# Kernel optimization log

Hardware: AMD Instinct MI355X
Metric: run time of the kernel (lower is better)

The kernel has to match this reference:

```python
import jax, jax.numpy as jnp
import numpy as np

L = 8192
E = 1024
H = 16
D = E // H  # head_dim = 64


def setup_inputs() -> dict:
    key = jax.random.key(0)
    ks = jax.random.split(key, 5)
    x = jax.random.normal(ks[0], (L, E), dtype=jnp.float32)
    in_proj_weight = jax.random.normal(ks[1], (3 * E, E), dtype=jnp.float32) * (1.0 / np.sqrt(E))
    in_proj_bias = jax.random.normal(ks[2], (3 * E,), dtype=jnp.float32) * 0.02
    out_proj_weight = jax.random.normal(ks[3], (E, E), dtype=jnp.float32) * (1.0 / np.sqrt(E))
    out_proj_bias = jax.random.normal(ks[4], (E,), dtype=jnp.float32) * 0.02
    return {
        "x": x,
        "in_proj_weight": in_proj_weight,
        "in_proj_bias": in_proj_bias,
        "out_proj_weight": out_proj_weight,
        "out_proj_bias": out_proj_bias,
    }


def reference(x, in_proj_weight, in_proj_bias, out_proj_weight, out_proj_bias):
    # Single-token query (decode-style): q from x[:1], k/v from full sequence.
    q = x[:1] @ in_proj_weight[:E].T + in_proj_bias[:E]            # [1, E]
    k = x @ in_proj_weight[E:2 * E].T + in_proj_bias[E:2 * E]      # [L, E]
    v = x @ in_proj_weight[2 * E:].T + in_proj_bias[2 * E:]        # [L, E]

    q = q.reshape(1, H, D).transpose(1, 0, 2)   # [H, 1, D]
    k = k.reshape(L, H, D).transpose(1, 2, 0)   # [H, D, L]
    v = v.reshape(L, H, D).transpose(1, 0, 2)   # [H, L, D]

    scale = 1.0 / np.sqrt(D).astype(np.float32)
    dot = jnp.matmul(q, k) * scale              # [H, 1, L]
    attn = jax.nn.softmax(dot, axis=-1)
    out = jnp.matmul(attn, v)                   # [H, 1, D]
    out = out.transpose(1, 0, 2).reshape(1, E)  # [1, E]
    return out @ out_proj_weight.T + out_proj_bias
```

## Files before the change

### kernel.cpp

```cpp
#include <hip/hip_runtime.h>
#include <hip/hip_bf16.h>

#define LSEQ 8192
#define E 1024
#define H 16

typedef __attribute__((ext_vector_type(8))) short short8;
typedef __attribute__((ext_vector_type(4))) float f32x4;

__device__ inline unsigned short f2bf(float f) {
    union { float f; unsigned int i; } v; v.f = f;
    unsigned int x = v.i;
    unsigned int r = (x + 0x7fffu + ((x >> 16) & 1u)) >> 16;
    return (unsigned short)r;
}

__device__ inline float wave_reduce_sum(float v) {
    #pragma unroll
    for (int off = 32; off > 0; off >>= 1) v += __shfl_xor(v, off, 64);
    return v;
}

__global__ __launch_bounds__(256) void k0_q(
    const float* __restrict__ x, const float* __restrict__ W,
    const float* __restrict__ bias, float* __restrict__ q_ws)
{
    int wave = threadIdx.x >> 6, lane = threadIdx.x & 63;
    int i = blockIdx.x * 4 + wave;
    const f32x4* wp = (const f32x4*)(W + i * E) + lane * 4;
    const f32x4* xp = (const f32x4*)(x) + lane * 4;
    float s = 0.f;
    #pragma unroll
    for (int j = 0; j < 4; j++) {
        f32x4 w4 = wp[j], x4 = xp[j];
        s += w4[0] * x4[0] + w4[1] * x4[1] + w4[2] * x4[2] + w4[3] * x4[3];
    }
    s = wave_reduce_sum(s);
    if (lane == 0) q_ws[i] = s + bias[i];
}

__global__ __launch_bounds__(256) void k1_rc(
    const float* __restrict__ W, const float* __restrict__ bias,
    const float* __restrict__ q_ws, unsigned short* __restrict__ r_bf,
    float* __restrict__ c_ws)
{
    __shared__ float red[4][64];
    int hb = blockIdx.x >> 4, ec = blockIdx.x & 15;
    int lane = threadIdx.x & 63, wq = threadIdx.x >> 6;
    int e = ec * 64 + lane;
    const float* qh = q_ws + hb * 64;
    float acc = 0.f;
    #pragma unroll
    for (int i = 0; i < 16; i++) {
        int d = wq * 16 + i;
        acc += qh[d] * W[(E + hb * 64 + d) * E + e];
    }
    red[wq][lane] = acc;
    __syncthreads();
    if (wq == 0) {
        float s = red[0][lane] + red[1][lane] + red[2][lane] + red[3][lane];
        r_bf[hb * E + e] = f2bf(s * 0.125f);
    }
    if (ec == 0 && wq == 1) {
        float v = qh[lane] * bias[E + hb * 64 + lane];
        v = wave_reduce_sum(v);
        if (lane == 0) c_ws[hb] = v * 0.125f;
    }
}

__global__ __launch_bounds__(256) void k2_scores(
    const float* __restrict__ x,
    const unsigned short* __restrict__ r_bf,
    const float* __restrict__ c_ws,
    float* __restrict__ scores)
{
    __shared__ f32x4 comb[2][64];
    int tid = threadIdx.x;
    int wave = tid >> 6, lane = tid & 63;
    int mloc = wave >> 1, khalf = wave & 1;
    int mtile = blockIdx.x * 2 + mloc;
    int mbase = mtile * 16;
    int rw = lane & 15, quad = lane >> 4;
    float cv = (khalf == 0) ? c_ws[rw] : 0.f;
    f32x4 acc = {cv, cv, cv, cv};
    const f32x4* ap = (const f32x4*)(x + (mbase + rw) * E + khalf * 512) + quad * 2;
    const short8* bp = (const short8*)(r_bf + rw * E + khalf * 512) + quad;
    #pragma unroll 4
    for (int kk = 0; kk < 16; kk++) {
        f32x4 a0 = ap[kk * 8];
        f32x4 a1 = ap[kk * 8 + 1];
        short8 af;
        af[0] = (short)f2bf(a0[0]); af[1] = (short)f2bf(a0[1]);
        af[2] = (short)f2bf(a0[2]); af[3] = (short)f2bf(a0[3]);
        af[4] = (short)f2bf(a1[0]); af[5] = (short)f2bf(a1[1]);
        af[6] = (short)f2bf(a1[2]); af[7] = (short)f2bf(a1[3]);
        short8 bfr = bp[kk * 4];
        acc = __builtin_amdgcn_mfma_f32_16x16x32_bf16(af, bfr, acc, 0, 0, 0);
    }
    if (khalf == 1) comb[mloc][lane] = acc;
    __syncthreads();
    if (khalf == 0) {
        f32x4 o = comb[mloc][lane];
        #pragma unroll
        for (int j = 0; j < 4; j++) {
            int m = mbase + quad * 4 + j;
            scores[rw * LSEQ + m] = acc[j] + o[j];
        }
    }
}

__global__ __launch_bounds__(256) void k3_stats(
    const float* __restrict__ scores, float* __restrict__ m_ws, float* __restrict__ is_ws)
{
    __shared__ float red[4];
    __shared__ float red2[4];
    int h = blockIdx.x, tid = threadIdx.x;
    const float* sp = scores + h * LSEQ;
    float mx = -1e30f;
    for (int i = tid; i < LSEQ; i += 256) mx = fmaxf(mx, sp[i]);
    #pragma unroll
    for (int off = 32; off > 0; off >>= 1) mx = fmaxf(mx, __shfl_xor(mx, off, 64));
    if ((tid & 63) == 0) red[tid >> 6] = mx;
    __syncthreads();
    mx = fmaxf(fmaxf(red[0], red[1]), fmaxf(red[2], red[3]));
    float sum = 0.f;
    for (int i = tid; i < LSEQ; i += 256) sum += __expf(sp[i] - mx);
    sum = wave_reduce_sum(sum);
    if ((tid & 63) == 0) red2[tid >> 6] = sum;
    __syncthreads();
    sum = red2[0] + red2[1] + red2[2] + red2[3];
    if (tid == 0) { m_ws[h] = mx; is_ws[h] = 1.f / sum; }
}

__global__ __launch_bounds__(256) void k4_partial(
    const float* __restrict__ x,
    const float* __restrict__ scores,
    const float* __restrict__ m_ws, const float* __restrict__ is_ws,
    float* __restrict__ partial, int rows_per_chunk)
{
    __shared__ float p_lds[64 * 16];
    __shared__ float sm[16], si[16];
    int b = blockIdx.x;
    int chunk = b >> 2, qc = b & 3;
    int tid = threadIdx.x;
    int lbase = chunk * rows_per_chunk;
    int e0 = qc * 256 + tid;
    if (tid < 16) { sm[tid] = m_ws[tid]; si[tid] = is_ws[tid]; }
    float acc[16];
    #pragma unroll
    for (int h = 0; h < 16; h++) acc[h] = 0.f;

    for (int t0 = 0; t0 < rows_per_chunk; t0 += 64) {
        __syncthreads();
        #pragma unroll
        for (int j = 0; j < 4; j++) {
            int idx = tid * 4 + j;
            int li = idx >> 4, hh = idx & 15;
            float sc = scores[hh * LSEQ + lbase + t0 + li];
            p_lds[idx] = __expf(sc - sm[hh]) * si[hh];
        }
        __syncthreads();
        #pragma unroll 8
        for (int li = 0; li < 64; li++) {
            float xv = x[(lbase + t0 + li) * E + e0];
            const f32x4* pp = (const f32x4*)&p_lds[li * 16];
            #pragma unroll
            for (int g = 0; g < 4; g++) {
                f32x4 pv = pp[g];
                acc[g * 4 + 0] += pv[0] * xv;
                acc[g * 4 + 1] += pv[1] * xv;
                acc[g * 4 + 2] += pv[2] * xv;
                acc[g * 4 + 3] += pv[3] * xv;
            }
        }
    }
    #pragma unroll
    for (int h = 0; h < 16; h++) partial[(chunk * 16 + h) * E + e0] = acc[h];
}

__global__ __launch_bounds__(256) void k4b_reduce(
    const float* __restrict__ partial, float* __restrict__ y, int nchunk)
{
    __shared__ float red[4][64];
    int lane = threadIdx.x & 63, cq = threadIdx.x >> 6;
    int o = blockIdx.x * 64 + lane;
    float s = 0.f;
    for (int c = cq; c < nchunk; c += 4) s += partial[c * (H * E) + o];
    red[cq][lane] = s;
    __syncthreads();
    if (cq == 0) y[o] = red[0][lane] + red[1][lane] + red[2][lane] + red[3][lane];
}

__global__ __launch_bounds__(256) void k5a_oh(
    const float* __restrict__ W, const float* __restrict__ bias,
    const float* __restrict__ y, float* __restrict__ oh)
{
    int wave = threadIdx.x >> 6, lane = threadIdx.x & 63;
    int i = blockIdx.x * 4 + wave;
    int h = i >> 6;
    const f32x4* wp = (const f32x4*)(W + (2 * E + i) * E) + lane * 4;
    const f32x4* yp = (const f32x4*)(y + h * E) + lane * 4;
    float s = 0.f;
    #pragma unroll
    for (int j = 0; j < 4; j++) {
        f32x4 w4 = wp[j], y4 = yp[j];
        s += w4[0] * y4[0] + w4[1] * y4[1] + w4[2] * y4[2] + w4[3] * y4[3];
    }
    s = wave_reduce_sum(s);
    if (lane == 0) oh[i] = s + bias[2 * E + i];
}

__global__ __launch_bounds__(256) void k5b_out(
    const float* __restrict__ Wout, const float* __restrict__ bout,
    const float* __restrict__ oh, float* __restrict__ out)
{
    int wave = threadIdx.x >> 6, lane = threadIdx.x & 63;
    int j = blockIdx.x * 4 + wave;
    const f32x4* wp = (const f32x4*)(Wout + j * E) + lane * 4;
    const f32x4* op = (const f32x4*)(oh) + lane * 4;
    float s = 0.f;
    #pragma unroll
    for (int jj = 0; jj < 4; jj++) {
        f32x4 w4 = wp[jj], o4 = op[jj];
        s += w4[0] * o4[0] + w4[1] * o4[1] + w4[2] * o4[2] + w4[3] * o4[3];
    }
    s = wave_reduce_sum(s);
    if (lane == 0) out[j] = s + bout[j];
}

extern "C" void kernel_launch(void* const* d_in, const int* in_sizes, int n_in,
                              void* d_out, int out_size, void* d_ws, size_t ws_size,
                              hipStream_t stream) {
    const float* x  = (const float*)d_in[0];
    const float* W  = (const float*)d_in[1];
    const float* b  = (const float*)d_in[2];
    const float* Wo = (const float*)d_in[3];
    const float* bo = (const float*)d_in[4];
    float* out = (float*)d_out;
    char* ws = (char*)d_ws;

    float* q_ws  = (float*)(ws);
    float* c_ws  = (float*)(ws + 4096);
    float* m_ws  = (float*)(ws + 4160);
    float* is_ws = (float*)(ws + 4224);
    float* oh_ws = (float*)(ws + 4352);
    unsigned short* r_bf = (unsigned short*)(ws + 8448);
    float* scores = (float*)(ws + 8448 + 32768);
    float* y_ws   = (float*)(ws + 41216 + 524288);
    float* partial = (float*)(ws + 565504 + 65536);

    int nchunk = 64;
    while (nchunk > 4 && (size_t)631040 + (size_t)nchunk * 65536 > ws_size) nchunk >>= 1;
    int rows_per_chunk = LSEQ / nchunk;

    hipLaunchKernelGGL(k0_q,      dim3(256), dim3(256), 0, stream, x, W, b, q_ws);
    hipLaunchKernelGGL(k1_rc,     dim3(256), dim3(256), 0, stream, W, b, q_ws, r_bf, c_ws);
    hipLaunchKernelGGL(k2_scores, dim3(256), dim3(256), 0, stream, x, r_bf, c_ws, scores);
    hipLaunchKernelGGL(k3_stats,  dim3(16),  dim3(256), 0, stream, scores, m_ws, is_ws);
    hipLaunchKernelGGL(k4_partial,dim3(nchunk * 4), dim3(256), 0, stream,
                       x, scores, m_ws, is_ws, partial, rows_per_chunk);
    hipLaunchKernelGGL(k4b_reduce,dim3(256), dim3(256), 0, stream, partial, y_ws, nchunk);
    hipLaunchKernelGGL(k5a_oh,    dim3(256), dim3(256), 0, stream, W, b, y_ws, oh_ws);
    hipLaunchKernelGGL(k5b_out,   dim3(256), dim3(256), 0, stream, Wo, bo, oh_ws, out);
}
```

Baseline: 133.8 us.

## Fuse all attention stages into one cooperative persistent kernel with unnormalized softmax

Replaces the eight separate kernel launches with a single cooperative kernel of 256 blocks that separates the stages with grid.sync. The scores are no longer written to global memory. Each block loads 32 rows of x into LDS once and uses them for both the score MFMA and the weighted value accumulation. Softmax skips max subtraction: exp(s) is accumulated and normalized by a global atomic sum at the output-projection stage. This removes launch overheads, the scores round trip and the second pass over x, but it risks exp overflow with no max subtraction and depends on ws_size being large enough for 256 partials.

Result: slower. 261.5 us (+95.4%).

```diff
diff --git a/kernel.cpp b/kernel.cpp
--- a/kernel.cpp
+++ b/kernel.cpp
@@ -1,5 +1,7 @@
 #include <hip/hip_runtime.h>
-#include <hip/hip_bf16.h>
+#include <hip/hip_cooperative_groups.h>
+
+namespace cg = cooperative_groups;
 
 #define LSEQ 8192
 #define E 1024
@@ -11,8 +13,7 @@
 __device__ inline unsigned short f2bf(float f) {
     union { float f; unsigned int i; } v; v.f = f;
     unsigned int x = v.i;
-    unsigned int r = (x + 0x7fffu + ((x >> 16) & 1u)) >> 16;
-    return (unsigned short)r;
+    return (unsigned short)((x + 0x7fffu + ((x >> 16) & 1u)) >> 16);
 }
 
 __device__ inline float wave_reduce_sum(float v) {
@@ -21,211 +22,193 @@
     return v;
 }
 
-__global__ __launch_bounds__(256) void k0_q(
+__global__ __launch_bounds__(512, 1) void fused_mha(
     const float* __restrict__ x, const float* __restrict__ W,
-    const float* __restrict__ bias, float* __restrict__ q_ws)
+    const float* __restrict__ b, const float* __restrict__ Wo,
+    const float* __restrict__ bo,
+    float* __restrict__ q_ws, unsigned short* __restrict__ r_bf,
+    float* __restrict__ c_ws, float* __restrict__ S_ws,
+    float* __restrict__ partial, float* __restrict__ u_ws,
+    float* __restrict__ oh_ws, float* __restrict__ out)
 {
-    int wave = threadIdx.x >> 6, lane = threadIdx.x & 63;
-    int i = blockIdx.x * 4 + wave;
-    const f32x4* wp = (const f32x4*)(W + i * E) + lane * 4;
-    const f32x4* xp = (const f32x4*)(x) + lane * 4;
-    float s = 0.f;
-    #pragma unroll
-    for (int j = 0; j < 4; j++) {
-        f32x4 w4 = wp[j], x4 = xp[j];
-        s += w4[0] * x4[0] + w4[1] * x4[1] + w4[2] * x4[2] + w4[3] * x4[3];
-    }
-    s = wave_reduce_sum(s);
-    if (lane == 0) q_ws[i] = s + bias[i];
-}
-
-__global__ __launch_bounds__(256) void k1_rc(
-    const float* __restrict__ W, const float* __restrict__ bias,
-    const float* __restrict__ q_ws, unsigned short* __restrict__ r_bf,
-    float* __restrict__ c_ws)
-{
-    __shared__ float red[4][64];
-    int hb = blockIdx.x >> 4, ec = blockIdx.x & 15;
-    int lane = threadIdx.x & 63, wq = threadIdx.x >> 6;
-    int e = ec * 64 + lane;
-    const float* qh = q_ws + hb * 64;
-    float acc = 0.f;
-    #pragma unroll
-    for (int i = 0; i < 16; i++) {
-        int d = wq * 16 + i;
-        acc += qh[d] * W[(E + hb * 64 + d) * E + e];
-    }
-    red[wq][lane] = acc;
-    __syncthreads();
-    if (wq == 0) {
-        float s = red[0][lane] + red[1][lane] + red[2][lane] + red[3][lane];
-        r_bf[hb * E + e] = f2bf(s * 0.125f);
-    }
-    if (ec == 0 && wq == 1) {
-        float v = qh[lane] * bias[E + hb * 64 + lane];
-        v = wave_reduce_sum(v);
-        if (lane == 0) c_ws[hb] = v * 0.125f;
-    }
-}
-
-__global__ __launch_bounds__(256) void k2_scores(
-    const float* __restrict__ x,
-    const unsigned short* __restrict__ r_bf,
-    const float* __restrict__ c_ws,
-    float* __restrict__ scores)
-{
-    __shared__ f32x4 comb[2][64];
-    int tid = threadIdx.x;
-    int wave = tid >> 6, lane = tid & 63;
-    int mloc = wave >> 1, khalf = wave & 1;
-    int mtile = blockIdx.x * 2 + mloc;
-    int mbase = mtile * 16;
-    int rw = lane & 15, quad = lane >> 4;
-    float cv = (khalf == 0) ? c_ws[rw] : 0.f;
-    f32x4 acc = {cv, cv, cv, cv};
-    const f32x4* ap = (const f32x4*)(x + (mbase + rw) * E + khalf * 512) + quad * 2;
-    const short8* bp = (const short8*)(r_bf + rw * E + khalf * 512) + quad;
-    #pragma unroll 4
-    for (int kk = 0; kk < 16; kk++) {
-        f32x4 a0 = ap[kk * 8];
-        f32x4 a1 = ap[kk * 8 + 1];
-        short8 af;
-        af[0] = (short)f2bf(a0[0]); af[1] = (short)f2bf(a0[1]);
-        af[2] = (short)f2bf(a0[2]); af[3] = (short)f2bf(a0[3]);
-        af[4] = (short)f2bf(a1[0]); af[5] = (short)f2bf(a1[1]);
-        af[6] = (short)f2bf(a1[2]); af[7] = (short)f2bf(a1[3]);
-        short8 bfr = bp[kk * 4];
-        acc = __builtin_amdgcn_mfma_f32_16x16x32_bf16(af, bfr, acc, 0, 0, 0);
-    }
-    if (khalf == 1) comb[mloc][lane] = acc;
-    __syncthreads();
-    if (khalf == 0) {
-        f32x4 o = comb[mloc][lane];
+    cg::grid_group grid = cg::this_grid();
+    __shared__ float x_lds[16 * 1028];
+    __shared__ float sp[8 * 64 * 4];
+    __shared__ float p_lds[16 * 16];
+    __shared__ float esum[16];
+    __shared__ float red[8 * 64];
+
+    const int tid  = threadIdx.x;
+    const int wave = tid >> 6, lane = tid & 63;
+    const int beta = blockIdx.x;
+
+    if (wave < 4) {
+        int i = beta * 4 + wave;
+        const f32x4* wp = (const f32x4*)(W + i * E) + lane * 4;
+        const f32x4* xp = (const f32x4*)(x) + lane * 4;
+        float s = 0.f;
         #pragma unroll
         for (int j = 0; j < 4; j++) {
-            int m = mbase + quad * 4 + j;
-            scores[rw * LSEQ + m] = acc[j] + o[j];
-        }
-    }
-}
-
-__global__ __launch_bounds__(256) void k3_stats(
-    const float* __restrict__ scores, float* __restrict__ m_ws, float* __restrict__ is_ws)
-{
-    __shared__ float red[4];
-    __shared__ float red2[4];
-    int h = blockIdx.x, tid = threadIdx.x;
-    const float* sp = scores + h * LSEQ;
-    float mx = -1e30f;
-    for (int i = tid; i < LSEQ; i += 256) mx = fmaxf(mx, sp[i]);
-    #pragma unroll
-    for (int off = 32; off > 0; off >>= 1) mx = fmaxf(mx, __shfl_xor(mx, off, 64));
-    if ((tid & 63) == 0) red[tid >> 6] = mx;
-    __syncthreads();
-    mx = fmaxf(fmaxf(red[0], red[1]), fmaxf(red[2], red[3]));
-    float sum = 0.f;
-    for (int i = tid; i < LSEQ; i += 256) sum += __expf(sp[i] - mx);
-    sum = wave_reduce_sum(sum);
-    if ((tid & 63) == 0) red2[tid >> 6] = sum;
-    __syncthreads();
-    sum = red2[0] + red2[1] + red2[2] + red2[3];
-    if (tid == 0) { m_ws[h] = mx; is_ws[h] = 1.f / sum; }
-}
-
-__global__ __launch_bounds__(256) void k4_partial(
-    const float* __restrict__ x,
-    const float* __restrict__ scores,
-    const float* __restrict__ m_ws, const float* __restrict__ is_ws,
-    float* __restrict__ partial, int rows_per_chunk)
-{
-    __shared__ float p_lds[64 * 16];
-    __shared__ float sm[16], si[16];
-    int b = blockIdx.x;
-    int chunk = b >> 2, qc = b & 3;
-    int tid = threadIdx.x;
-    int lbase = chunk * rows_per_chunk;
-    int e0 = qc * 256 + tid;
-    if (tid < 16) { sm[tid] = m_ws[tid]; si[tid] = is_ws[tid]; }
-    float acc[16];
-    #pragma unroll
-    for (int h = 0; h < 16; h++) acc[h] = 0.f;
-
-    for (int t0 = 0; t0 < rows_per_chunk; t0 += 64) {
+            f32x4 w4 = wp[j], x4 = xp[j];
+            s += w4[0]*x4[0] + w4[1]*x4[1] + w4[2]*x4[2] + w4[3]*x4[3];
+        }
+        s = wave_reduce_sum(s);
+        if (lane == 0) q_ws[i] = s + b[i];
+    } else if (wave == 4 && beta == 0 && lane < 16) {
+        S_ws[lane] = 0.f;
+    }
+    grid.sync();
+
+    {
+        int hb = beta >> 4, ec = beta & 15;
+        int e = ec * 64 + lane;
+        const float* qh = q_ws + hb * 64;
+        float acc = 0.f;
+        #pragma unroll
+        for (int i = 0; i < 8; i++) {
+            int d = wave * 8 + i;
+            acc += qh[d] * W[(E + hb * 64 + d) * E + e];
+        }
+        red[wave * 64 + lane] = acc;
         __syncthreads();
+        if (wave == 0) {
+            float s = 0.f;
+            #pragma unroll
+            for (int w = 0; w < 8; w++) s += red[w * 64 + lane];
+            r_bf[hb * E + e] = f2bf(s * 0.125f);
+        }
+        if (ec == 0 && wave == 1) {
+            float v = qh[lane] * b[E + hb * 64 + lane];
+            v = wave_reduce_sum(v);
+            if (lane == 0) c_ws[hb] = v * 0.125f;
+        }
+    }
+    grid.sync();
+
+    {
+        if (tid < 16) esum[tid] = 0.f;
+        float acc[32];
+        #pragma unroll
+        for (int i = 0; i < 32; i++) acc[i] = 0.f;
+        int lbase = beta * 32;
+
+        for (int t = 0; t < 2; t++) {
+            int R0 = lbase + t * 16;
+            __syncthreads();
+            {
+                int row = tid >> 5, ch = tid & 31;
+                const f32x4* src = (const f32x4*)(x + (R0 + row) * E);
+                float* dst = x_lds + row * 1028;
+                #pragma unroll
+                for (int j = 0; j < 8; j++) {
+                    int c4 = ch + 32 * j;
+                    *(f32x4*)(dst + c4 * 4) = src[c4];
+                }
+            }
+            __syncthreads();
+            {
+                int rw = lane & 15, quad = lane >> 4;
+                f32x4 sacc = {0.f, 0.f, 0.f, 0.f};
+                const float* arow = x_lds + rw * 1028 + wave * 128 + quad * 8;
+                const short8* bp = (const short8*)(r_bf + rw * E + wave * 128 + quad * 8);
+                #pragma unroll
+                for (int kk = 0; kk < 4; kk++) {
+                    f32x4 a0 = *(const f32x4*)(arow + kk * 32);
+                    f32x4 a1 = *(const f32x4*)(arow + kk * 32 + 4);
+                    short8 af;
+                    af[0] = (short)f2bf(a0[0]); af[1] = (short)f2bf(a0[1]);
+                    af[2] = (short)f2bf(a0[2]); af[3] = (short)f2bf(a0[3]);
+                    af[4] = (short)f2bf(a1[0]); af[5] = (short)f2bf(a1[1]);
+                    af[6] = (short)f2bf(a1[2]); af[7] = (short)f2bf(a1[3]);
+                    short8 bfr = bp[kk * 4];
+                    sacc = __builtin_amdgcn_mfma_f32_16x16x32_bf16(af, bfr, sacc, 0, 0, 0);
+                }
+                *(f32x4*)&sp[(wave * 64 + lane) * 4] = sacc;
+            }
+            __syncthreads();
+            if (tid < 256) {
+                int m = tid >> 4, h = tid & 15;
+                int ln = (m >> 2) * 16 + h, rg = m & 3;
+                float s = c_ws[h];
+                #pragma unroll
+                for (int w = 0; w < 8; w++) s += sp[(w * 64 + ln) * 4 + rg];
+                float p = __expf(s);
+                p_lds[m * 16 + h] = p;
+                atomicAdd(&esum[h], p);
+            }
+            __syncthreads();
+            #pragma unroll 4
+            for (int m = 0; m < 16; m++) {
+                float2 xv = *(const float2*)&x_lds[m * 1028 + tid * 2];
+                const f32x4* pp = (const f32x4*)&p_lds[m * 16];
+                #pragma unroll
+                for (int g = 0; g < 4; g++) {
+                    f32x4 pv = pp[g];
+                    acc[(g * 4 + 0) * 2 + 0] += pv[0] * xv.x;
+                    acc[(g * 4 + 0) * 2 + 1] += pv[0] * xv.y;
+                    acc[(g * 4 + 1) * 2 + 0] += pv[1] * xv.x;
+                    acc[(g * 4 + 1) * 2 + 1] += pv[1] * xv.y;
+                    acc[(g * 4 + 2) * 2 + 0] += pv[2] * xv.x;
+                    acc[(g * 4 + 2) * 2 + 1] += pv[2] * xv.y;
+                    acc[(g * 4 + 3) * 2 + 0] += pv[3] * xv.x;
+                    acc[(g * 4 + 3) * 2 + 1] += pv[3] * xv.y;
+                }
+            }
+        }
+        __syncthreads();
+        #pragma unroll
+        for (int h = 0; h < 16; h++) {
+            float2 v; v.x = acc[h * 2]; v.y = acc[h * 2 + 1];
+            *(float2*)&partial[(beta * 16 + h) * E + tid * 2] = v;
+        }
+        if (tid < 16) atomicAdd(&S_ws[tid], esum[tid]);
+    }
+    grid.sync();
+
+    {
+        int o = beta * 64 + lane;
+        float s = 0.f;
+        for (int bb = wave; bb < 256; bb += 8) s += partial[bb * (H * E) + o];
+        red[wave * 64 + lane] = s;
+        __syncthreads();
+        if (wave == 0) {
+            float tot = 0.f;
+            #pragma unroll
+            for (int w = 0; w < 8; w++) tot += red[w * 64 + lane];
+            u_ws[o] = tot;
+        }
+    }
+    grid.sync();
+
+    if (wave < 4) {
+        int i = beta * 4 + wave;
+        int h = i >> 6;
+        const f32x4* wp = (const f32x4*)(W + (2 * E + i) * E) + lane * 4;
+        const f32x4* up = (const f32x4*)(u_ws + h * E) + lane * 4;
+        float s = 0.f;
         #pragma unroll
         for (int j = 0; j < 4; j++) {
-            int idx = tid * 4 + j;
-            int li = idx >> 4, hh = idx & 15;
-            float sc = scores[hh * LSEQ + lbase + t0 + li];
-            p_lds[idx] = __expf(sc - sm[hh]) * si[hh];
-        }
-        __syncthreads();
-        #pragma unroll 8
-        for (int li = 0; li < 64; li++) {
-            float xv = x[(lbase + t0 + li) * E + e0];
-            const f32x4* pp = (const f32x4*)&p_lds[li * 16];
-            #pragma unroll
-            for (int g = 0; g < 4; g++) {
-                f32x4 pv = pp[g];
-                acc[g * 4 + 0] += pv[0] * xv;
-                acc[g * 4 + 1] += pv[1] * xv;
-                acc[g * 4 + 2] += pv[2] * xv;
-                acc[g * 4 + 3] += pv[3] * xv;
-            }
-        }
-    }
-    #pragma unroll
-    for (int h = 0; h < 16; h++) partial[(chunk * 16 + h) * E + e0] = acc[h];
-}
-
-__global__ __launch_bounds__(256) void k4b_reduce(
-    const float* __restrict__ partial, float* __restrict__ y, int nchunk)
-{
-    __shared__ float red[4][64];
-    int lane = threadIdx.x & 63, cq = threadIdx.x >> 6;
-    int o = blockIdx.x * 64 + lane;
-    float s = 0.f;
-    for (int c = cq; c < nchunk; c += 4) s += partial[c * (H * E) + o];
-    red[cq][lane] = s;
-    __syncthreads();
-    if (cq == 0) y[o] = red[0][lane] + red[1][lane] + red[2][lane] + red[3][lane];
-}
-
-__global__ __launch_bounds__(256) void k5a_oh(
-    const float* __restrict__ W, const float* __restrict__ bias,
-    const float* __restrict__ y, float* __restrict__ oh)
-{
-    int wave = threadIdx.x >> 6, lane = threadIdx.x & 63;
-    int i = blockIdx.x * 4 + wave;
-    int h = i >> 6;
-    const f32x4* wp = (const f32x4*)(W + (2 * E + i) * E) + lane * 4;
-    const f32x4* yp = (const f32x4*)(y + h * E) + lane * 4;
-    float s = 0.f;
-    #pragma unroll
-    for (int j = 0; j < 4; j++) {
-        f32x4 w4 = wp[j], y4 = yp[j];
-        s += w4[0] * y4[0] + w4[1] * y4[1] + w4[2] * y4[2] + w4[3] * y4[3];
-    }
-    s = wave_reduce_sum(s);
-    if (lane == 0) oh[i] = s + bias[2 * E + i];
-}
-
-__global__ __launch_bounds__(256) void k5b_out(
-    const float* __restrict__ Wout, const float* __restrict__ bout,
-    const float* __restrict__ oh, float* __restrict__ out)
-{
-    int wave = threadIdx.x >> 6, lane = threadIdx.x & 63;
-    int j = blockIdx.x * 4 + wave;
-    const f32x4* wp = (const f32x4*)(Wout + j * E) + lane * 4;
-    const f32x4* op = (const f32x4*)(oh) + lane * 4;
-    float s = 0.f;
-    #pragma unroll
-    for (int jj = 0; jj < 4; jj++) {
-        f32x4 w4 = wp[jj], o4 = op[jj];
-        s += w4[0] * o4[0] + w4[1] * o4[1] + w4[2] * o4[2] + w4[3] * o4[3];
-    }
-    s = wave_reduce_sum(s);
-    if (lane == 0) out[j] = s + bout[j];
+            f32x4 w4 = wp[j], u4 = up[j];
+            s += w4[0]*u4[0] + w4[1]*u4[1] + w4[2]*u4[2] + w4[3]*u4[3];
+        }
+        s = wave_reduce_sum(s);
+        if (lane == 0) oh_ws[i] = s / S_ws[h] + b[2 * E + i];
+    }
+    grid.sync();
+
+    if (wave < 4) {
+        int j = beta * 4 + wave;
+        const f32x4* wp = (const f32x4*)(Wo + j * E) + lane * 4;
+        const f32x4* op = (const f32x4*)(oh_ws) + lane * 4;
+        float s = 0.f;
+        #pragma unroll
+        for (int jj = 0; jj < 4; jj++) {
+            f32x4 w4 = wp[jj], o4 = op[jj];
+            s += w4[0]*o4[0] + w4[1]*o4[1] + w4[2]*o4[2] + w4[3]*o4[3];
+        }
+        s = wave_reduce_sum(s);
+        if (lane == 0) out[j] = s + bo[j];
+    }
 }
 
 extern "C" void kernel_launch(void* const* d_in, const int* in_sizes, int n_in,
@@ -241,25 +224,17 @@
 
     float* q_ws  = (float*)(ws);
     float* c_ws  = (float*)(ws + 4096);
-    float* m_ws  = (float*)(ws + 4160);
-    float* is_ws = (float*)(ws + 4224);
+    float* S_ws  = (float*)(ws + 4224);
     float* oh_ws = (float*)(ws + 4352);
     unsigned short* r_bf = (unsigned short*)(ws + 8448);
-    float* scores = (float*)(ws + 8448 + 32768);
-    float* y_ws   = (float*)(ws + 41216 + 524288);
-    float* partial = (float*)(ws + 565504 + 65536);
-
-    int nchunk = 64;
-    while (nchunk > 4 && (size_t)631040 + (size_t)nchunk * 65536 > ws_size) nchunk >>= 1;
-    int rows_per_chunk = LSEQ / nchunk;
-
-    hipLaunchKernelGGL(k0_q,      dim3(256), dim3(256), 0, stream, x, W, b, q_ws);
-    hipLaunchKernelGGL(k1_rc,     dim3(256), dim3(256), 0, stream, W, b, q_ws, r_bf, c_ws);
-    hipLaunchKernelGGL(k2_scores, dim3(256), dim3(256), 0, stream, x, r_bf, c_ws, scores);
-    hipLaunchKernelGGL(k3_stats,  dim3(16),  dim3(256), 0, stream, scores, m_ws, is_ws);
-    hipLaunchKernelGGL(k4_partial,dim3(nchunk * 4), dim3(256), 0, stream,
-                       x, scores, m_ws, is_ws, partial, rows_per_chunk);
-    hipLaunchKernelGGL(k4b_reduce,dim3(256), dim3(256), 0, stream, partial, y_ws, nchunk);
-    hipLaunchKernelGGL(k5a_oh,    dim3(256), dim3(256), 0, stream, W, b, y_ws, oh_ws);
-    hipLaunchKernelGGL(k5b_out,   dim3(256), dim3(256), 0, stream, Wo, bo, oh_ws, out);
-}
+    float* u_ws  = (float*)(ws + 41216);
+    float* partial = (float*)(ws + 106752);
+
+    void* args[] = {
+        (void*)&x, (void*)&W, (void*)&b, (void*)&Wo, (void*)&bo,
+        (void*)&q_ws, (void*)&r_bf, (void*)&c_ws, (void*)&S_ws,
+        (void*)&partial, (void*)&u_ws, (void*)&oh_ws, (void*)&out
+    };
+    hipLaunchCooperativeKernel((const void*)fused_mha, dim3(256), dim3(512),
+                               args, 0, stream);
+}
```
